# Optimization experiments

Hardware: AMD Instinct MI355X
Metric: run time of the kernel (lower is better)

Reference implementation:

```python
import jax, jax.numpy as jnp
import numpy as np

B = 1024        # number of graphs
MAXLEN = 64     # max nodes per graph (pad_sequence length)
E = 256         # hidden_size
H = 8           # num_heads
HD = E // H     # head dim
NEG = -1e9


def setup_inputs() -> dict:
    key = jax.random.key(0)
    k0, k1, k2 = jax.random.split(key, 3)
    lens = np.tile(np.array([32, 48, 64, 40], dtype=np.int64), B // 4)  # sum = 47104
    batch_indices = jnp.asarray(np.repeat(np.arange(B, dtype=np.int64), lens))
    N = int(lens.sum())
    node_features = jax.random.normal(k0, (N, E), dtype=jnp.float32)
    in_proj_w = jax.random.normal(k1, (3 * E, E), dtype=jnp.float32) * (1.0 / np.sqrt(E))
    in_proj_b = jnp.zeros((3 * E,), dtype=jnp.float32)
    out_proj_w = jax.random.normal(k2, (E, E), dtype=jnp.float32) * (1.0 / np.sqrt(E))
    out_proj_b = jnp.zeros((E,), dtype=jnp.float32)
    return {"node_features": node_features, "batch_indices": batch_indices,
            "in_proj_w": in_proj_w, "in_proj_b": in_proj_b,
            "out_proj_w": out_proj_w, "out_proj_b": out_proj_b}


def _pad_ragged(node_features, batch_indices):
    # counts per graph, start offset of each graph, position of each node in its graph
    N = node_features.shape[0]
    counts = jax.ops.segment_sum(jnp.ones((N,), jnp.int32), batch_indices, num_segments=B)
    starts = jnp.cumsum(counts) - counts
    pos = jnp.arange(N) - starts[batch_indices]
    padded = jnp.zeros((B, MAXLEN, E), node_features.dtype).at[batch_indices, pos].set(node_features)
    key_pad = jnp.arange(MAXLEN)[None, :] >= counts[:, None]  # [B, L] True = padding
    return padded, key_pad


def reference(node_features, batch_indices, in_proj_w, in_proj_b, out_proj_w, out_proj_b):
    padded, key_pad = _pad_ragged(node_features, batch_indices)   # [B,L,E], [B,L]
    qkv = padded @ in_proj_w.T + in_proj_b                        # [B,L,3E]
    q, k, v = jnp.split(qkv, 3, axis=-1)
    q = q.reshape(B, MAXLEN, H, HD)
    k = k.reshape(B, MAXLEN, H, HD)
    v = v.reshape(B, MAXLEN, H, HD)
    scores = jnp.einsum('blhd,bmhd->bhlm', q, k) / jnp.sqrt(jnp.float32(HD))
    scores = jnp.where(key_pad[:, None, None, :], NEG, scores)    # mask padded keys
    attn = jax.nn.softmax(scores, axis=-1)                        # [B,H,L,L]
    ctx = jnp.einsum('bhlm,bmhd->blhd', attn, v).reshape(B, MAXLEN, E)
    out = ctx @ out_proj_w.T + out_proj_b                         # [B,L,E]
    out = jnp.transpose(out, (1, 0, 2))                           # [L,B,E] seq-first like torch
    weights = attn.mean(axis=1)                                   # [B,L,L] head-averaged
    return out, weights
```

## Files before the change

### kernel.cpp

```cpp
#include <hip/hip_runtime.h>

typedef unsigned short u16;
typedef short bf16x8 __attribute__((ext_vector_type(8)));
typedef float f32x4 __attribute__((ext_vector_type(4)));

#define MFMA16(a, b, c) __builtin_amdgcn_mfma_f32_16x16x32_bf16((a), (b), (c), 0, 0, 0)

__device__ u16 g_q[1024 * 8 * 64 * 32];
__device__ u16 g_k[1024 * 8 * 64 * 32];
__device__ u16 g_vt[1024 * 8 * 32 * 64];

static __device__ __forceinline__ u16 f2bf(float f) {
    union { float f; unsigned int u; } v; v.f = f;
    unsigned int u = v.u;
    u += 0x7fffu + ((u >> 16) & 1u);
    return (u16)(u >> 16);
}

__global__ void prep_kernel(const int* __restrict__ bidx, int N,
                            const float* __restrict__ X,
                            const float* __restrict__ w_in, const float* __restrict__ w_out,
                            int* __restrict__ starts, int* __restrict__ counts,
                            u16* __restrict__ w_in_bf, u16* __restrict__ w_out_bf,
                            u16* __restrict__ xbf) {
    int tid = blockIdx.x * blockDim.x + threadIdx.x;
    if (tid < 1024) {
        int lo = 0, hi = N;
        while (lo < hi) { int mid = (lo + hi) >> 1; if (bidx[mid] < tid) lo = mid + 1; else hi = mid; }
        int s0 = lo;
        lo = 0; hi = N;
        int v1 = tid + 1;
        while (lo < hi) { int mid = (lo + hi) >> 1; if (bidx[mid] < v1) lo = mid + 1; else hi = mid; }
        starts[tid] = s0;
        counts[tid] = lo - s0;
    }
    {
        float4 v = ((const float4*)w_in)[tid];
        ushort4 o; o.x = f2bf(v.x); o.y = f2bf(v.y); o.z = f2bf(v.z); o.w = f2bf(v.w);
        ((ushort4*)w_in_bf)[tid] = o;
    }
    if (tid < 16384) {
        float4 v = ((const float4*)w_out)[tid];
        ushort4 o; o.x = f2bf(v.x); o.y = f2bf(v.y); o.z = f2bf(v.z); o.w = f2bf(v.w);
        ((ushort4*)w_out_bf)[tid] = o;
    }
    if (xbf) {
        int total = N * 32;
        for (int i = tid; i < total; i += 49152) {
            float4 v0 = ((const float4*)X)[2 * i];
            float4 v1 = ((const float4*)X)[2 * i + 1];
            bf16x8 o;
            o[0] = (short)f2bf(v0.x); o[1] = (short)f2bf(v0.y);
            o[2] = (short)f2bf(v0.z); o[3] = (short)f2bf(v0.w);
            o[4] = (short)f2bf(v1.x); o[5] = (short)f2bf(v1.y);
            o[6] = (short)f2bf(v1.z); o[7] = (short)f2bf(v1.w);
            ((bf16x8*)xbf)[i] = o;
        }
    }
}

__global__ __launch_bounds__(256, 2) void qkv_kernel(
    const float* __restrict__ X, const u16* __restrict__ xbf,
    const float* __restrict__ bias_in,
    const int* __restrict__ starts, const int* __restrict__ counts,
    const u16* __restrict__ w_in_bf) {

    const int b = blockIdx.x;
    const int tid = threadIdx.x;
    const int w = tid >> 6;
    const int lane = tid & 63;
    const int n = lane & 15;
    const int quad = lane >> 4;
    const int s = starts[b];
    const int c = counts[b];

    bf16x8 afr[4][8];
    #pragma unroll
    for (int st = 0; st < 4; ++st) {
        const int row = st * 16 + n;
        const bool ok = row < c;
        if (xbf) {
            const u16* src = xbf + (long)(s + row) * 256 + quad * 8;
            #pragma unroll
            for (int ks = 0; ks < 8; ++ks) {
                bf16x8 a = (bf16x8){0, 0, 0, 0, 0, 0, 0, 0};
                if (ok) a = *(const bf16x8*)(src + ks * 32);
                afr[st][ks] = a;
            }
        } else {
            const float* src = X + (long)(s + row) * 256 + quad * 8;
            #pragma unroll
            for (int ks = 0; ks < 8; ++ks) {
                float4 v0 = make_float4(0.f, 0.f, 0.f, 0.f);
                float4 v1 = make_float4(0.f, 0.f, 0.f, 0.f);
                if (ok) {
                    v0 = *(const float4*)(src + ks * 32);
                    v1 = *(const float4*)(src + ks * 32 + 4);
                }
                bf16x8 a;
                a[0] = (short)f2bf(v0.x); a[1] = (short)f2bf(v0.y);
                a[2] = (short)f2bf(v0.z); a[3] = (short)f2bf(v0.w);
                a[4] = (short)f2bf(v1.x); a[5] = (short)f2bf(v1.y);
                a[6] = (short)f2bf(v1.z); a[7] = (short)f2bf(v1.w);
                afr[st][ks] = a;
            }
        }
    }

    const int hw  = w >> 1;
    const int dlo = (w & 1) * 16;

    #pragma unroll 1
    for (int g = 0; g < 4; ++g) {
        for (int i = 0; i < 3; ++i) {
            const int wrow = i * 256 + g * 64 + w * 16 + n;
            const u16* wr = w_in_bf + wrow * 256 + quad * 8;
            const float bias = bias_in[wrow];

            bf16x8 bfr[8];
            #pragma unroll
            for (int ks = 0; ks < 8; ++ks) bfr[ks] = *(const bf16x8*)(wr + ks * 32);

            f32x4 acc[4];
            #pragma unroll
            for (int st = 0; st < 4; ++st) acc[st] = (f32x4){0.f, 0.f, 0.f, 0.f};
            #pragma unroll
            for (int ks = 0; ks < 8; ++ks)
                #pragma unroll
                for (int st = 0; st < 4; ++st)
                    acc[st] = MFMA16(afr[st][ks], bfr[ks], acc[st]);

            const int h = g * 2 + hw;
            if (i == 2) {
                u16* vd = g_vt + ((long)(b * 8 + h) * 32 + dlo + n) * 64;
                #pragma unroll
                for (int st = 0; st < 4; ++st) {
                    ushort4 pk;
                    pk.x = f2bf(acc[st][0] + bias); pk.y = f2bf(acc[st][1] + bias);
                    pk.z = f2bf(acc[st][2] + bias); pk.w = f2bf(acc[st][3] + bias);
                    *(ushort4*)&vd[st * 16 + quad * 4] = pk;
                }
            } else {
                u16* dst = (i == 0 ? g_q : g_k) + (long)(b * 8 + h) * 2048;
                #pragma unroll
                for (int st = 0; st < 4; ++st)
                    #pragma unroll
                    for (int r = 0; r < 4; ++r)
                        dst[(st * 16 + quad * 4 + r) * 32 + dlo + n] = f2bf(acc[st][r] + bias);
            }
        }
    }
}

__global__ __launch_bounds__(512, 4) void attn_kernel(
    const float* __restrict__ bias_out, const int* __restrict__ counts,
    const u16* __restrict__ w_out_bf,
    float* __restrict__ out, float* __restrict__ wout) {

    __shared__ u16 p_s[8][16][72];
    __shared__ u16 cs[64][264];

    const int b = blockIdx.x;
    const int tid = threadIdx.x;
    const int w = tid >> 6;
    const int lane = tid & 63;
    const int n = lane & 15;
    const int quad = lane >> 4;
    const int c = counts[b];

    const int hh = w & 1;
    const int rt = w >> 1;
    const int m0 = rt * 16;

    const float scale = 0.17677669529663687f;
    float wacc[4][4];
    #pragma unroll
    for (int t = 0; t < 4; ++t)
        #pragma unroll
        for (int r = 0; r < 4; ++r) wacc[t][r] = 0.f;

    #pragma unroll 1
    for (int g = 0; g < 4; ++g) {
        const int h = g * 2 + hh;
        const u16* qh = g_q  + (long)(b * 8 + h) * 2048;
        const u16* kh = g_k  + (long)(b * 8 + h) * 2048;
        const u16* vh = g_vt + (long)(b * 8 + h) * 2048;

        bf16x8 aq = *(const bf16x8*)&qh[(m0 + n) * 32 + quad * 8];
        f32x4 sc[4];
        #pragma unroll
        for (int t = 0; t < 4; ++t) {
            bf16x8 bk = *(const bf16x8*)&kh[(t * 16 + n) * 32 + quad * 8];
            f32x4 z = (f32x4){0.f, 0.f, 0.f, 0.f};
            sc[t] = MFMA16(bk, aq, z);
        }
        float pv[4][4];
        float mx = -1e30f;
        #pragma unroll
        for (int t = 0; t < 4; ++t)
            #pragma unroll
            for (int r = 0; r < 4; ++r) {
                float sv = ((t * 16 + quad * 4 + r) < c) ? sc[t][r] * scale : -1e30f;
                pv[t][r] = sv;
                mx = fmaxf(mx, sv);
            }
        mx = fmaxf(mx, __shfl_xor(mx, 16, 64));
        mx = fmaxf(mx, __shfl_xor(mx, 32, 64));
        float sm = 0.f;
        #pragma unroll
        for (int t = 0; t < 4; ++t)
            #pragma unroll
            for (int r = 0; r < 4; ++r) {
                float e = ((t * 16 + quad * 4 + r) < c) ? __expf(pv[t][r] - mx) : 0.f;
                pv[t][r] = e; sm += e;
            }
        sm += __shfl_xor(sm, 16, 64);
        sm += __shfl_xor(sm, 32, 64);
        float invs = 1.f / sm;
        #pragma unroll
        for (int t = 0; t < 4; ++t)
            #pragma unroll
            for (int r = 0; r < 4; ++r) {
                pv[t][r] *= invs;
                wacc[t][r] += pv[t][r] * 0.125f;
            }
        #pragma unroll
        for (int t = 0; t < 4; ++t) {
            ushort4 pk;
            pk.x = f2bf(pv[t][0]); pk.y = f2bf(pv[t][1]);
            pk.z = f2bf(pv[t][2]); pk.w = f2bf(pv[t][3]);
            *(ushort4*)&p_s[w][n][t * 16 + quad * 4] = pk;
        }
        #pragma unroll
        for (int nt = 0; nt < 2; ++nt) {
            f32x4 acc = (f32x4){0.f, 0.f, 0.f, 0.f};
            #pragma unroll
            for (int k2 = 0; k2 < 2; ++k2) {
                bf16x8 ap = *(const bf16x8*)&p_s[w][n][k2 * 32 + quad * 8];
                bf16x8 bv = *(const bf16x8*)&vh[(nt * 16 + n) * 64 + k2 * 32 + quad * 8];
                acc = MFMA16(ap, bv, acc);
            }
            #pragma unroll
            for (int r = 0; r < 4; ++r)
                cs[m0 + quad * 4 + r][h * 32 + nt * 16 + n] = f2bf(acc[r]);
        }
    }
    __syncthreads();

    {
        float* pw = (float*)&p_s[w & ~1][0][0];
        if (hh == 0) {
            #pragma unroll
            for (int t = 0; t < 4; ++t) {
                float4 f4 = make_float4(wacc[t][0], wacc[t][1], wacc[t][2], wacc[t][3]);
                *(float4*)&pw[n * 72 + t * 16 + quad * 4] = f4;
            }
        }
        __syncthreads();
        if (hh == 1) {
            #pragma unroll
            for (int t = 0; t < 4; ++t) {
                float4 f4 = *(const float4*)&pw[n * 72 + t * 16 + quad * 4];
                float4 o;
                o.x = wacc[t][0] + f4.x; o.y = wacc[t][1] + f4.y;
                o.z = wacc[t][2] + f4.z; o.w = wacc[t][3] + f4.w;
                *(float4*)&wout[b * 4096 + (m0 + n) * 64 + t * 16 + quad * 4] = o;
            }
        }
    }

    {
        const int sp = w & 3;
        const int cq = w >> 2;
        bf16x8 actx[8];
        #pragma unroll
        for (int ks = 0; ks < 8; ++ks)
            actx[ks] = *(const bf16x8*)&cs[sp * 16 + n][ks * 32 + quad * 8];

        #pragma unroll 2
        for (int ci = 0; ci < 8; ++ci) {
            const int ct = cq * 8 + ci;
            const u16* wr = w_out_bf + (ct * 16 + n) * 256 + quad * 8;
            f32x4 acc = (f32x4){0.f, 0.f, 0.f, 0.f};
            #pragma unroll
            for (int kh = 0; kh < 2; ++kh) {
                bf16x8 bfr[4];
                #pragma unroll
                for (int k4 = 0; k4 < 4; ++k4) bfr[k4] = *(const bf16x8*)(wr + (kh * 4 + k4) * 32);
                #pragma unroll
                for (int k4 = 0; k4 < 4; ++k4) acc = MFMA16(actx[kh * 4 + k4], bfr[k4], acc);
            }
            const float bias = bias_out[ct * 16 + n];
            const int orow = sp * 16 + quad * 4;
            #pragma unroll
            for (int r = 0; r < 4; ++r)
                out[(orow + r) * 262144 + b * 256 + ct * 16 + n] = acc[r] + bias;
        }
    }
}

extern "C" void kernel_launch(void* const* d_in, const int* in_sizes, int n_in,
                              void* d_out, int out_size, void* d_ws, size_t ws_size,
                              hipStream_t stream) {
    const float* X     = (const float*)d_in[0];
    const int*   bidx  = (const int*)d_in[1];
    const float* w_in  = (const float*)d_in[2];
    const float* b_in  = (const float*)d_in[3];
    const float* w_out = (const float*)d_in[4];
    const float* b_out = (const float*)d_in[5];
    const int N = in_sizes[1];

    float* out  = (float*)d_out;
    float* wout = out + 64 * 1024 * 256;

    int* starts   = (int*)d_ws;
    int* counts   = starts + 1024;
    u16* w_in_bf  = (u16*)(counts + 1024);
    u16* w_out_bf = w_in_bf + 196608;
    u16* xbf      = w_out_bf + 65536;

    const size_t base_need = 2048ull * 4 + 196608ull * 2 + 65536ull * 2;
    const size_t xbf_bytes = (size_t)N * 256 * 2;
    if (ws_size < base_need + xbf_bytes) xbf = nullptr;

    hipLaunchKernelGGL(prep_kernel, dim3(192), dim3(256), 0, stream,
                       bidx, N, X, w_in, w_out, starts, counts, w_in_bf, w_out_bf, xbf);
    hipLaunchKernelGGL(qkv_kernel, dim3(1024), dim3(256), 0, stream,
                       X, xbf, b_in, starts, counts, w_in_bf);
    hipLaunchKernelGGL(attn_kernel, dim3(1024), dim3(512), 0, stream,
                       b_out, counts, w_out_bf, out, wout);
}
```

Before: 298.4 us.

## Widen QKV blocks to eight waves and prefetch next-head Q/K/V in attention

The QKV projection kernel now runs 512 threads per block, with eight waves sharing the 48 weight tiles through a flattened loop instead of four waves doing 12 tiles each. The attention kernel loads Q, K and V fragments for the next head while the current head is processed, hiding global load latency. The prep kernel launch grows to 512 blocks, with a guard on the weight conversion and a larger stride for the activation conversion loop. In exchange, each QKV wave still loads the full activation tile, so activation reads per block double. The tighter register budget at 512 threads may also cause spills.

After: 307.7 us. 3.1% more time.

```diff
diff --git a/kernel.cpp b/kernel.cpp
--- a/kernel.cpp
+++ b/kernel.cpp
@@ -34,7 +34,7 @@
         starts[tid] = s0;
         counts[tid] = lo - s0;
     }
-    {
+    if (tid < 49152) {
         float4 v = ((const float4*)w_in)[tid];
         ushort4 o; o.x = f2bf(v.x); o.y = f2bf(v.y); o.z = f2bf(v.z); o.w = f2bf(v.w);
         ((ushort4*)w_in_bf)[tid] = o;
@@ -46,7 +46,7 @@
     }
     if (xbf) {
         int total = N * 32;
-        for (int i = tid; i < total; i += 49152) {
+        for (int i = tid; i < total; i += 131072) {
             float4 v0 = ((const float4*)X)[2 * i];
             float4 v1 = ((const float4*)X)[2 * i + 1];
             bf16x8 o;
@@ -59,7 +59,7 @@
     }
 }
 
-__global__ __launch_bounds__(256, 2) void qkv_kernel(
+__global__ __launch_bounds__(512, 2) void qkv_kernel(
     const float* __restrict__ X, const u16* __restrict__ xbf,
     const float* __restrict__ bias_in,
     const int* __restrict__ starts, const int* __restrict__ counts,
@@ -107,47 +107,48 @@
         }
     }
 
-    const int hw  = w >> 1;
-    const int dlo = (w & 1) * 16;
-
     #pragma unroll 1
-    for (int g = 0; g < 4; ++g) {
-        for (int i = 0; i < 3; ++i) {
-            const int wrow = i * 256 + g * 64 + w * 16 + n;
-            const u16* wr = w_in_bf + wrow * 256 + quad * 8;
-            const float bias = bias_in[wrow];
-
-            bf16x8 bfr[8];
-            #pragma unroll
-            for (int ks = 0; ks < 8; ++ks) bfr[ks] = *(const bf16x8*)(wr + ks * 32);
-
-            f32x4 acc[4];
-            #pragma unroll
-            for (int st = 0; st < 4; ++st) acc[st] = (f32x4){0.f, 0.f, 0.f, 0.f};
-            #pragma unroll
-            for (int ks = 0; ks < 8; ++ks)
+    for (int it = 0; it < 6; ++it) {
+        const int idx = w + it * 8;
+        const int g = idx / 12;
+        const int j = idx - g * 12;
+        const int type = j >> 2;
+        const int sub = j & 3;
+        const int wrow = type * 256 + g * 64 + sub * 16 + n;
+        const u16* wr = w_in_bf + wrow * 256 + quad * 8;
+        const float bias = bias_in[wrow];
+
+        bf16x8 bfr[8];
+        #pragma unroll
+        for (int ks = 0; ks < 8; ++ks) bfr[ks] = *(const bf16x8*)(wr + ks * 32);
+
+        f32x4 acc[4];
+        #pragma unroll
+        for (int st = 0; st < 4; ++st) acc[st] = (f32x4){0.f, 0.f, 0.f, 0.f};
+        #pragma unroll
+        for (int ks = 0; ks < 8; ++ks)
+            #pragma unroll
+            for (int st = 0; st < 4; ++st)
+                acc[st] = MFMA16(afr[st][ks], bfr[ks], acc[st]);
+
+        const int h = g * 2 + (sub >> 1);
+        const int dlo = (sub & 1) * 16;
+        if (type == 2) {
+            u16* vd = g_vt + ((long)(b * 8 + h) * 32 + dlo + n) * 64;
+            #pragma unroll
+            for (int st = 0; st < 4; ++st) {
+                ushort4 pk;
+                pk.x = f2bf(acc[st][0] + bias); pk.y = f2bf(acc[st][1] + bias);
+                pk.z = f2bf(acc[st][2] + bias); pk.w = f2bf(acc[st][3] + bias);
+                *(ushort4*)&vd[st * 16 + quad * 4] = pk;
+            }
+        } else {
+            u16* dst = (type == 0 ? g_q : g_k) + (long)(b * 8 + h) * 2048;
+            #pragma unroll
+            for (int st = 0; st < 4; ++st)
                 #pragma unroll
-                for (int st = 0; st < 4; ++st)
-                    acc[st] = MFMA16(afr[st][ks], bfr[ks], acc[st]);
-
-            const int h = g * 2 + hw;
-            if (i == 2) {
-                u16* vd = g_vt + ((long)(b * 8 + h) * 32 + dlo + n) * 64;
-                #pragma unroll
-                for (int st = 0; st < 4; ++st) {
-                    ushort4 pk;
-                    pk.x = f2bf(acc[st][0] + bias); pk.y = f2bf(acc[st][1] + bias);
-                    pk.z = f2bf(acc[st][2] + bias); pk.w = f2bf(acc[st][3] + bias);
-                    *(ushort4*)&vd[st * 16 + quad * 4] = pk;
-                }
-            } else {
-                u16* dst = (i == 0 ? g_q : g_k) + (long)(b * 8 + h) * 2048;
-                #pragma unroll
-                for (int st = 0; st < 4; ++st)
-                    #pragma unroll
-                    for (int r = 0; r < 4; ++r)
-                        dst[(st * 16 + quad * 4 + r) * 32 + dlo + n] = f2bf(acc[st][r] + bias);
-            }
+                for (int r = 0; r < 4; ++r)
+                    dst[(st * 16 + quad * 4 + r) * 32 + dlo + n] = f2bf(acc[st][r] + bias);
         }
     }
 }
@@ -171,6 +172,7 @@
     const int hh = w & 1;
     const int rt = w >> 1;
     const int m0 = rt * 16;
+    const long bh = (long)b * 8;
 
     const float scale = 0.17677669529663687f;
     float wacc[4][4];
@@ -179,20 +181,36 @@
         #pragma unroll
         for (int r = 0; r < 4; ++r) wacc[t][r] = 0.f;
 
+    bf16x8 aq, bk[4], bv[4];
+    {
+        const u16* qh = g_q  + (bh + hh) * 2048;
+        const u16* kh = g_k  + (bh + hh) * 2048;
+        const u16* vh = g_vt + (bh + hh) * 2048;
+        aq = *(const bf16x8*)&qh[(m0 + n) * 32 + quad * 8];
+        #pragma unroll
+        for (int t = 0; t < 4; ++t)
+            bk[t] = *(const bf16x8*)&kh[(t * 16 + n) * 32 + quad * 8];
+        #pragma unroll
+        for (int j = 0; j < 4; ++j)
+            bv[j] = *(const bf16x8*)&vh[((j >> 1) * 16 + n) * 64 + (j & 1) * 32 + quad * 8];
+    }
+
     #pragma unroll 1
     for (int g = 0; g < 4; ++g) {
         const int h = g * 2 + hh;
-        const u16* qh = g_q  + (long)(b * 8 + h) * 2048;
-        const u16* kh = g_k  + (long)(b * 8 + h) * 2048;
-        const u16* vh = g_vt + (long)(b * 8 + h) * 2048;
-
-        bf16x8 aq = *(const bf16x8*)&qh[(m0 + n) * 32 + quad * 8];
         f32x4 sc[4];
         #pragma unroll
         for (int t = 0; t < 4; ++t) {
-            bf16x8 bk = *(const bf16x8*)&kh[(t * 16 + n) * 32 + quad * 8];
             f32x4 z = (f32x4){0.f, 0.f, 0.f, 0.f};
-            sc[t] = MFMA16(bk, aq, z);
+            sc[t] = MFMA16(bk[t], aq, z);
+        }
+        if (g < 3) {
+            const u16* qh = g_q + (bh + h + 2) * 2048;
+            const u16* kh = g_k + (bh + h + 2) * 2048;
+            aq = *(const bf16x8*)&qh[(m0 + n) * 32 + quad * 8];
+            #pragma unroll
+            for (int t = 0; t < 4; ++t)
+                bk[t] = *(const bf16x8*)&kh[(t * 16 + n) * 32 + quad * 8];
         }
         float pv[4][4];
         float mx = -1e30f;
@@ -231,18 +249,25 @@
             pk.z = f2bf(pv[t][2]); pk.w = f2bf(pv[t][3]);
             *(ushort4*)&p_s[w][n][t * 16 + quad * 4] = pk;
         }
+        bf16x8 ap[2];
+        #pragma unroll
+        for (int k2 = 0; k2 < 2; ++k2)
+            ap[k2] = *(const bf16x8*)&p_s[w][n][k2 * 32 + quad * 8];
         #pragma unroll
         for (int nt = 0; nt < 2; ++nt) {
             f32x4 acc = (f32x4){0.f, 0.f, 0.f, 0.f};
             #pragma unroll
-            for (int k2 = 0; k2 < 2; ++k2) {
-                bf16x8 ap = *(const bf16x8*)&p_s[w][n][k2 * 32 + quad * 8];
-                bf16x8 bv = *(const bf16x8*)&vh[(nt * 16 + n) * 64 + k2 * 32 + quad * 8];
-                acc = MFMA16(ap, bv, acc);
-            }
+            for (int k2 = 0; k2 < 2; ++k2)
+                acc = MFMA16(ap[k2], bv[nt * 2 + k2], acc);
             #pragma unroll
             for (int r = 0; r < 4; ++r)
                 cs[m0 + quad * 4 + r][h * 32 + nt * 16 + n] = f2bf(acc[r]);
+        }
+        if (g < 3) {
+            const u16* vh = g_vt + (bh + h + 2) * 2048;
+            #pragma unroll
+            for (int j = 0; j < 4; ++j)
+                bv[j] = *(const bf16x8*)&vh[((j >> 1) * 16 + n) * 64 + (j & 1) * 32 + quad * 8];
         }
     }
     __syncthreads();
@@ -323,9 +348,9 @@
     const size_t xbf_bytes = (size_t)N * 256 * 2;
     if (ws_size < base_need + xbf_bytes) xbf = nullptr;
 
-    hipLaunchKernelGGL(prep_kernel, dim3(192), dim3(256), 0, stream,
+    hipLaunchKernelGGL(prep_kernel, dim3(512), dim3(256), 0, stream,
                        bidx, N, X, w_in, w_out, starts, counts, w_in_bf, w_out_bf, xbf);
-    hipLaunchKernelGGL(qkv_kernel, dim3(1024), dim3(256), 0, stream,
+    hipLaunchKernelGGL(qkv_kernel, dim3(1024), dim3(512), 0, stream,
                        X, xbf, b_in, starts, counts, w_in_bf);
     hipLaunchKernelGGL(attn_kernel, dim3(1024), dim3(512), 0, stream,
                        b_out, counts, w_out_bf, out, wout);
```
